# Performance work log

Hardware: AMD Instinct MI355X
Metric: run time of the kernel (lower is better)

## Reference

```python
import jax, jax.numpy as jnp
import numpy as np

B, N, L, C = 4, 16, 192, 64
H = 128
ROW, COL = 16, 12  # L == ROW*COL, ROW >= COL
NUM = 2  # class_num


def setup_inputs() -> dict:
    key = jax.random.key(0)
    ks = jax.random.split(key, 12)
    s = 1.0 / np.sqrt(H).astype(np.float32)
    u = lambda k, shape: jax.random.uniform(k, shape, jnp.float32, -s, s)
    return {
        "x": jax.random.normal(ks[0], (B, N, L, C), jnp.float32),
        "pad_mask": jnp.ones((B, N), jnp.bool_),
        "fc3_w": u(ks[1], (H, C)), "fc3_b": u(ks[2], (H,)),
        "fc4_w": u(ks[3], (H, H)), "fc4_b": u(ks[4], (H,)),
        "W_enc": u(ks[5], (NUM, 6 * H, 3 * H)), "B_enc": u(ks[6], (NUM, 6 * H)),
        "fc1_w": u(ks[7], (NUM, 1, H)), "fc1_b": u(ks[8], (NUM, 1)),
        "fc2_w": u(ks[9], (NUM, 1, H)), "fc2_b": u(ks[10], (NUM, 1)),
    }


def _witran_encoder(a, W, Bb):
    # a: [COL*BN, slice_len, H] diagonally-shifted input; W: [6H, 3H]; Bb: [6H]
    RBN, slice_len, _ = a.shape
    BN = RBN // COL
    R = COL  # Water2sea_slice_num (after permute(2,0,1,3), slices run over col)
    slice_ids = jnp.arange(RBN) // BN
    xs = jnp.transpose(a, (1, 0, 2))  # [slice_len, RBN, H]

    def step(carry, inp):
        h_row, h_col = carry
        x_s, s = inp
        g = jnp.concatenate([h_row, h_col, x_s], axis=-1) @ W.T  # [RBN, 6H]
        # torch adds bias only to first batch*(s+1) rows, and only while s < slice_num
        mask = (slice_ids <= s) & (s < R)
        g = g + jnp.where(mask[:, None], Bb, jnp.zeros((), g.dtype))
        sig = jax.nn.sigmoid(g[:, : 4 * H])
        th = jnp.tanh(g[:, 4 * H:])
        u_r, o_r, u_c, o_c = jnp.split(sig, 4, axis=-1)
        i_r, i_c = jnp.split(th, 2, axis=-1)
        h_row = jnp.tanh((1 - u_r) * h_row + u_r * i_r) * o_r
        h_col = jnp.tanh((1 - u_c) * h_col + u_c * i_c) * o_c
        # saved pieces (only valid for late s; we keep the last, which is always valid)
        loc = jnp.clip(s - ROW + 1, 0, R - 1)
        row_save = jax.lax.dynamic_slice_in_dim(h_row, loc * BN, BN, axis=0)
        col_save = h_col[(R - 1) * BN:, :]  # save BEFORE roll, as in torch
        h_col = jnp.roll(h_col, BN, axis=0)
        return (h_row, h_col), (row_save, col_save)

    h0 = jnp.zeros((RBN, H), a.dtype)
    (_, _), (row_saves, col_saves) = jax.lax.scan(
        step, (h0, h0), (xs, jnp.arange(slice_len)))
    # last entries == hidden_row_all[:, -1, -1, :], hidden_col_all[:, -1, -1, :]
    return row_saves[-1], col_saves[-1]  # each [BN, H]


def reference(x, pad_mask, fc3_w, fc3_b, fc4_w, fc4_b, W_enc, B_enc,
              fc1_w, fc1_b, fc2_w, fc2_b):
    Bn, Nn = x.shape[0], x.shape[1]
    h = jax.nn.relu(x @ fc3_w.T + fc3_b) @ fc4_w.T + fc4_b  # [B,N,L,H]
    xr = h.reshape(-1, ROW, COL, H)          # [BN, row, col, H]
    inp = jnp.transpose(xr, (2, 0, 1, 3))    # [col, BN, row, H]
    slice_len = COL + ROW - 1
    # diagonal 'water2sea' shift: transfer[r, :, r:r+ROW] = inp[r]
    padded = jnp.pad(inp, ((0, 0), (0, 0), (0, COL - 1), (0, 0)))
    transfer = jax.vmap(lambda t, r: jnp.roll(t, r, axis=1))(padded, jnp.arange(COL))
    a = transfer.reshape(COL * Bn * Nn, slice_len, H)

    def per_class(W, Bb, f1w, f1b, f2w, f2b):
        row_last, col_last = _witran_encoder(a, W, Bb)
        # torch: row := hidden_col_all tail, col := hidden_row_all tail
        out = 0.5 * (col_last @ f1w.T + f1b) + 0.5 * (row_last @ f2w.T + f2b)
        return out[:, 0]  # [BN]

    y = jax.vmap(per_class)(W_enc, B_enc, fc1_w, fc1_b, fc2_w, fc2_b)  # [NUM, BN]
    return jnp.transpose(y).reshape(Bn, Nn, NUM)
```

## Files before the change

### kernel.cpp

```cpp
#include <hip/hip_runtime.h>

typedef _Float16 hf;
typedef _Float16 half2v __attribute__((ext_vector_type(2)));
typedef _Float16 half8 __attribute__((ext_vector_type(8)));
typedef float f32x4 __attribute__((ext_vector_type(4)));
typedef int int4v __attribute__((ext_vector_type(4)));

constexpr int Steps = 27;

constexpr int OFF_WX = 393216;
constexpr int OFF_F3 = 589824;
constexpr int OFF_F4 = 598016;
constexpr int OFF_XW = 614400;
constexpr int GST = 7;

__device__ __forceinline__ int aidx(int r, int k) {
  int blk = k >> 3;
  return r * 256 + (((blk ^ (r & 7)) & 31) << 3) + (k & 7);
}
__device__ __forceinline__ int hidx(int r, int k) {
  int blk = k >> 3;
  return r * 128 + (((blk ^ (r & 15)) & 15) << 3) + (k & 7);
}
__device__ __forceinline__ int xidx(int r, int k) {
  int blk = k >> 3;
  return r * 64 + (((blk ^ (r & 7)) & 7) << 3) + (k & 7);
}
__device__ __forceinline__ float sigmoidf_(float x) { return 1.0f / (1.0f + __expf(-x)); }
__device__ __forceinline__ float tanh_(float x) { return 1.0f - 2.0f / (__expf(2.0f * x) + 1.0f); }

__global__ __launch_bounds__(512) void prep(const float* __restrict__ fc3_w,
                                            const float* __restrict__ fc4_w,
                                            const float* __restrict__ W_enc,
                                            hf* __restrict__ wsh) {
  int idx = blockIdx.x * 512 + threadIdx.x;
  if (idx >= OFF_XW) return;
  float v;
  if (idx < OFF_WX) {
    int jj = idx & 7, lane = (idx >> 3) & 63, rest = idx >> 9;
    int ks = rest & 7; rest >>= 3;
    int j = rest % 3; rest /= 3;
    int wv = rest & 15, cls = rest >> 4;
    int gate = (wv < 8) ? (j < 2 ? j : 4) : (j < 2 ? j + 2 : 5);
    int n = gate * 128 + (wv & 7) * 16 + (lane & 15);
    int k = ks * 32 + ((lane >> 4) << 3) + jj;
    v = W_enc[(cls * 768 + n) * 384 + k];
  } else if (idx < OFF_F3) {
    int f = idx - OFF_WX;
    int j = f & 7, lane = (f >> 3) & 63, rest = f >> 9;
    int ks = rest & 3; rest >>= 2;
    int wv = rest & 7; rest >>= 3;
    int gate = rest % 6, cls = rest / 6;
    int n = gate * 128 + wv * 16 + (lane & 15);
    int k = 256 + ks * 32 + ((lane >> 4) << 3) + j;
    v = W_enc[(cls * 768 + n) * 384 + k];
  } else if (idx < OFF_F4) {
    int f = idx - OFF_F3;
    int j = f & 7, lane = (f >> 3) & 63, rest = f >> 9;
    int ks = rest & 1, wv = rest >> 1;
    int n = wv * 16 + (lane & 15), k = ks * 32 + ((lane >> 4) << 3) + j;
    v = fc3_w[n * 64 + k];
  } else {
    int f = idx - OFF_F4;
    int j = f & 7, lane = (f >> 3) & 63, rest = f >> 9;
    int ks = rest & 3, wv = rest >> 2;
    int n = wv * 16 + (lane & 15), k = ks * 32 + ((lane >> 4) << 3) + j;
    v = fc4_w[n * 128 + k];
  }
  wsh[idx] = (hf)v;
}

__global__ __launch_bounds__(512) void prelude(
    const float* __restrict__ x, const float* __restrict__ fc3_b, const float* __restrict__ fc4_b,
    const float* __restrict__ B_enc, const hf* __restrict__ wsh, hf* __restrict__ xWb) {
  const int t = threadIdx.x, lane = t & 63, wv = t >> 6;
  const int c16 = lane & 15, quad = lane >> 4;
  const int row0 = blockIdx.x * 64, bn = row0 / 192, l0 = row0 % 192;
  const int d = wv * 16 + c16;

  __shared__ __attribute__((aligned(16))) hf xA[64 * 64];
  __shared__ __attribute__((aligned(16))) hf hbuf[64 * 128];
  __shared__ __attribute__((aligned(16))) hf xout[64 * 768];
  __shared__ float actf[64];

  {
    int r = t >> 3, cb = (t & 7) * 8;
    const float* xp = x + (size_t)(row0 + r) * 64 + cb;
    f32x4 a = *(const f32x4*)xp, b = *(const f32x4*)(xp + 4);
    half8 h;
    h[0] = (hf)a.x; h[1] = (hf)a.y; h[2] = (hf)a.z; h[3] = (hf)a.w;
    h[4] = (hf)b.x; h[5] = (hf)b.y; h[6] = (hf)b.z; h[7] = (hf)b.w;
    *(half8*)&xA[xidx(r, cb)] = h;
  }
  if (t < 64) {
    int l = l0 + t;
    actf[t] = ((l / 12) + (l % 12)) < 12 ? 1.f : 0.f;
  }
  __syncthreads();

  {
    float b3v = fc3_b[d];
    half8 w0 = *(const half8*)(wsh + OFF_F3 + (wv * 2 + 0) * 512 + lane * 8);
    half8 w1 = *(const half8*)(wsh + OFF_F3 + (wv * 2 + 1) * 512 + lane * 8);
    f32x4 acc[4] = {{0, 0, 0, 0}, {0, 0, 0, 0}, {0, 0, 0, 0}, {0, 0, 0, 0}};
#pragma unroll
    for (int mt = 0; mt < 4; ++mt) {
      half8 a0 = *(const half8*)&xA[xidx(mt * 16 + c16, quad * 8)];
      half8 a1 = *(const half8*)&xA[xidx(mt * 16 + c16, 32 + quad * 8)];
      acc[mt] = __builtin_amdgcn_mfma_f32_16x16x32_f16(a0, w0, acc[mt], 0, 0, 0);
      acc[mt] = __builtin_amdgcn_mfma_f32_16x16x32_f16(a1, w1, acc[mt], 0, 0, 0);
    }
#pragma unroll
    for (int mt = 0; mt < 4; ++mt)
#pragma unroll
      for (int r = 0; r < 4; ++r)
        hbuf[hidx(mt * 16 + quad * 4 + r, d)] = (hf)fmaxf(acc[mt][r] + b3v, 0.f);
  }
  __syncthreads();

  {
    float b4v = fc4_b[d];
    half8 w4[4];
#pragma unroll
    for (int ks = 0; ks < 4; ++ks)
      w4[ks] = *(const half8*)(wsh + OFF_F4 + (wv * 4 + ks) * 512 + lane * 8);
    f32x4 acc[4] = {{0, 0, 0, 0}, {0, 0, 0, 0}, {0, 0, 0, 0}, {0, 0, 0, 0}};
#pragma unroll
    for (int mt = 0; mt < 4; ++mt)
#pragma unroll
      for (int ks = 0; ks < 4; ++ks) {
        half8 a = *(const half8*)&hbuf[hidx(mt * 16 + c16, ks * 32 + quad * 8)];
        acc[mt] = __builtin_amdgcn_mfma_f32_16x16x32_f16(a, w4[ks], acc[mt], 0, 0, 0);
      }
    __syncthreads();
#pragma unroll
    for (int mt = 0; mt < 4; ++mt)
#pragma unroll
      for (int r = 0; r < 4; ++r)
        hbuf[hidx(mt * 16 + quad * 4 + r, d)] = (hf)(acc[mt][r] + b4v);
  }
  __syncthreads();

  half8 af[4][4];
#pragma unroll
  for (int mt = 0; mt < 4; ++mt)
#pragma unroll
    for (int ks = 0; ks < 4; ++ks)
      af[mt][ks] = *(const half8*)&hbuf[hidx(mt * 16 + c16, ks * 32 + quad * 8)];

  for (int cls = 0; cls < 2; ++cls) {
    for (int g = 0; g < 6; ++g) {
      int pos = (g < 2) ? g : (g < 4 ? g + 1 : (g == 4 ? 2 : 5));
      half8 wf[4];
#pragma unroll
      for (int ks = 0; ks < 4; ++ks)
        wf[ks] = *(const half8*)(wsh + OFF_WX + (((cls * 6 + g) * 8 + wv) * 4 + ks) * 512 + lane * 8);
      float bv = B_enc[cls * 768 + g * 128 + d];
#pragma unroll
      for (int mt = 0; mt < 4; ++mt) {
        f32x4 acc = {0.f, 0.f, 0.f, 0.f};
#pragma unroll
        for (int ks = 0; ks < 4; ++ks)
          acc = __builtin_amdgcn_mfma_f32_16x16x32_f16(af[mt][ks], wf[ks], acc, 0, 0, 0);
#pragma unroll
        for (int r = 0; r < 4; ++r) {
          int row = mt * 16 + quad * 4 + r;
          xout[row * 768 + d * 6 + pos] = (hf)(acc[r] + actf[row] * bv);
        }
      }
    }
    __syncthreads();
    {
      const int* src = (const int*)xout;
      int* dst = (int*)(xWb + (((size_t)cls * 64 + bn) * 192 + l0) * 768);
#pragma unroll
      for (int i = 0; i < 12; ++i) {
        int base = (t + i * 512) * 4;
        *(int4v*)&dst[base] = *(const int4v*)&src[base];
      }
    }
    __syncthreads();
  }
}

__device__ __forceinline__ void xpre(const hf* __restrict__ xg, int t, int sN,
                                     unsigned* pa, unsigned* pb) {
#pragma unroll
  for (int i = 0; i < 3; ++i) {
    int u = t + (i << 10);
    int colf = u >= 1536;
    int q = colf ? u - 1536 : u;
    int c = q >> 7, dd = q & 127;
    int rr = sN - c;
    unsigned a = 0, b = 0;
    if (rr >= 0 && rr < 16) {
      const hf* p = xg + (size_t)(rr * 12 + c) * 768 + dd * 6;
      if (colf) {
        a = (unsigned)*(const unsigned short*)(p + 3);
        b = *(const unsigned*)(p + 4);
      } else {
        a = *(const unsigned*)p;
        b = (unsigned)*(const unsigned short*)(p + 2);
      }
    }
    pa[i] = a;
    pb[i] = b;
  }
}
__device__ __forceinline__ float lo16f(unsigned v) {
  return (float)__builtin_bit_cast(half2v, v)[0];
}
__device__ __forceinline__ float hi16f(unsigned v) {
  return (float)__builtin_bit_cast(half2v, v)[1];
}

__global__ __launch_bounds__(1024) __attribute__((amdgpu_waves_per_eu(4, 4))) void witran(
    const hf* __restrict__ wsh, const float* __restrict__ fc1_w, const float* __restrict__ fc1_b,
    const float* __restrict__ fc2_w, const float* __restrict__ fc2_b,
    const hf* __restrict__ xWb, float* __restrict__ out) {
  const int cls = blockIdx.x & 1, bn = blockIdx.x >> 1;
  const int t = threadIdx.x, lane = t & 63, wv = t >> 6;
  const int c16 = lane & 15, quad = lane >> 4;
  const int d = (wv & 7) * 16 + c16;
  const int goff = (wv < 8) ? 0 : 3;

  __shared__ __attribute__((aligned(16))) hf wlds[16 * 3072];
  __shared__ __attribute__((aligned(16))) hf A[2][4096];
  __shared__ float g_lds[12 * 128 * GST];
  __shared__ float red[128];

  for (int i = t; i < 4096; i += 1024) ((int*)A)[i] = 0;

  half8 wr[2][8], wr2[2];
  {
    const hf* wb = wsh + (((size_t)(cls * 16 + wv) * 3) * 8) * 512 + lane * 8;
#pragma unroll
    for (int ks = 0; ks < 8; ++ks) {
      wr[0][ks] = *(const half8*)(wb + ks * 512);
      wr[1][ks] = *(const half8*)(wb + (8 + ks) * 512);
    }
    wr2[0] = *(const half8*)(wb + 16 * 512);
    wr2[1] = *(const half8*)(wb + 17 * 512);
#pragma unroll
    for (int f = 0; f < 6; ++f)
      *(half8*)&wlds[wv * 3072 + f * 512 + lane * 8] = *(const half8*)(wb + (18 + f) * 512);
  }

  const hf* xg = xWb + ((size_t)cls * 64 + bn) * 192 * 768;

  unsigned pa[3], pb[3], na[3], nb[3];
  xpre(xg, t, 0, pa, pb);
  __syncthreads();

  for (int s = 0; s < Steps; ++s) {
    const hf* Ac = A[s & 1];
    hf* An = A[(s + 1) & 1];

    f32x4 a0 = {0, 0, 0, 0}, a1 = a0, a2 = a0;
#pragma unroll
    for (int ks = 0; ks < 8; ++ks) {
      half8 av = *(const half8*)&Ac[aidx(c16, ks * 32 + quad * 8)];
      a0 = __builtin_amdgcn_mfma_f32_16x16x32_f16(av, wr[0][ks], a0, 0, 0, 0);
      a1 = __builtin_amdgcn_mfma_f32_16x16x32_f16(av, wr[1][ks], a1, 0, 0, 0);
      half8 w2 = (ks < 2) ? wr2[ks]
                          : *(const half8*)&wlds[wv * 3072 + (ks - 2) * 512 + lane * 8];
      a2 = __builtin_amdgcn_mfma_f32_16x16x32_f16(av, w2, a2, 0, 0, 0);
    }
    if (quad < 3) {
#pragma unroll
      for (int r = 0; r < 4; ++r) {
        float* gp = &g_lds[((quad * 4 + r) * 128 + d) * GST + goff];
        gp[0] = a0[r];
        gp[1] = a1[r];
        gp[2] = a2[r];
      }
    }
    xpre(xg, t, s + 1, na, nb);
    __syncthreads();

#pragma unroll
    for (int i = 0; i < 3; ++i) {
      int u = t + (i << 10);
      int colf = u >= 1536;
      int q = colf ? u - 1536 : u;
      int c = q >> 7, dd = q & 127;
      if (c <= s) {
        const float* gp = &g_lds[(c * 128 + dd) * GST + (colf ? 3 : 0)];
        float xu, xo, xi;
        if (colf) {
          xu = lo16f(pa[i]); xo = lo16f(pb[i]); xi = hi16f(pb[i]);
        } else {
          xu = lo16f(pa[i]); xo = hi16f(pa[i]); xi = lo16f(pb[i]);
        }
        float gu = gp[0] + xu, go = gp[1] + xo, gi = gp[2] + xi;
        float hold = (float)Ac[aidx(c, colf ? 128 + dd : dd)];
        float uu = sigmoidf_(gu), oo = sigmoidf_(go), ii = tanh_(gi);
        float h = tanh_((1.f - uu) * hold + uu * ii) * oo;
        if (colf) {
          int c2 = (c == 11) ? 0 : c + 1;
          An[aidx(c2, 128 + dd)] = (hf)h;
        } else {
          An[aidx(c, dd)] = (hf)h;
        }
      }
    }
    __syncthreads();

#pragma unroll
    for (int i = 0; i < 3; ++i) { pa[i] = na[i]; pb[i] = nb[i]; }
  }

  if (t < 128) {
    float hr = (float)A[1][aidx(11, t)];
    float hc = (float)A[1][aidx(0, 128 + t)];
    red[t] = 0.5f * (hc * fc1_w[cls * 128 + t] + hr * fc2_w[cls * 128 + t]);
  }
  __syncthreads();
  if (t == 0) {
    float sum = 0.f;
    for (int i = 0; i < 128; ++i) sum += red[i];
    out[bn * 2 + cls] = sum + 0.5f * (fc1_b[cls] + fc2_b[cls]);
  }
}

extern "C" void kernel_launch(void* const* d_in, const int* in_sizes, int n_in,
                              void* d_out, int out_size, void* d_ws, size_t ws_size,
                              hipStream_t stream) {
  const float* x = (const float*)d_in[0];
  const float* fc3_w = (const float*)d_in[2];
  const float* fc3_b = (const float*)d_in[3];
  const float* fc4_w = (const float*)d_in[4];
  const float* fc4_b = (const float*)d_in[5];
  const float* W_enc = (const float*)d_in[6];
  const float* B_enc = (const float*)d_in[7];
  const float* fc1_w = (const float*)d_in[8];
  const float* fc1_b = (const float*)d_in[9];
  const float* fc2_w = (const float*)d_in[10];
  const float* fc2_b = (const float*)d_in[11];
  float* out = (float*)d_out;

  hf* wsh = (hf*)d_ws;
  hf* xWb = wsh + OFF_XW;

  prep<<<dim3(1200), dim3(512), 0, stream>>>(fc3_w, fc4_w, W_enc, wsh);
  prelude<<<dim3(192), dim3(512), 0, stream>>>(x, fc3_b, fc4_b, B_enc, wsh, xWb);
  witran<<<dim3(128), dim3(1024), 0, stream>>>(wsh, fc1_w, fc1_b, fc2_w, fc2_b, xWb, out);
}
```

Before: 194.9 us.

## Single-buffer hidden state, store gate pre-activations as fp16, move all third-gate weights to LDS

The hidden-state double buffer is replaced by a single buffer: each thread reads its old h into registers before the barrier and overwrites in place after it. Gate pre-activations are now staged in LDS as fp16 in a planar layout instead of fp32 with stride 7, which halves that traffic. All eight k-slices of the third weight set now come from LDS, so the wr2 registers go away. The next step's x prefetch is issued after the update instead of before the barrier. These changes cut LDS footprint and register pressure but add precision loss on the gates and make the prefetch latency less hidden.

After: 189.1 us. 3.0% less time.

```diff
diff --git a/kernel.cpp b/kernel.cpp
--- a/kernel.cpp
+++ b/kernel.cpp
@@ -12,7 +12,7 @@
 constexpr int OFF_F3 = 589824;
 constexpr int OFF_F4 = 598016;
 constexpr int OFF_XW = 614400;
-constexpr int GST = 7;
+constexpr int CST = 136;
 
 __device__ __forceinline__ int aidx(int r, int k) {
   int blk = k >> 3;
@@ -224,14 +224,14 @@
   const int d = (wv & 7) * 16 + c16;
   const int goff = (wv < 8) ? 0 : 3;
 
-  __shared__ __attribute__((aligned(16))) hf wlds[16 * 3072];
-  __shared__ __attribute__((aligned(16))) hf A[2][4096];
-  __shared__ float g_lds[12 * 128 * GST];
+  __shared__ __attribute__((aligned(16))) hf wlds[16 * 4096];
+  __shared__ __attribute__((aligned(16))) hf A[4096];
+  __shared__ hf g16[6 * 12 * CST];
   __shared__ float red[128];
 
-  for (int i = t; i < 4096; i += 1024) ((int*)A)[i] = 0;
-
-  half8 wr[2][8], wr2[2];
+  for (int i = t; i < 2048; i += 1024) ((int*)A)[i] = 0;
+
+  half8 wr[2][8];
   {
     const hf* wb = wsh + (((size_t)(cls * 16 + wv) * 3) * 8) * 512 + lane * 8;
 #pragma unroll
@@ -239,43 +239,45 @@
       wr[0][ks] = *(const half8*)(wb + ks * 512);
       wr[1][ks] = *(const half8*)(wb + (8 + ks) * 512);
     }
-    wr2[0] = *(const half8*)(wb + 16 * 512);
-    wr2[1] = *(const half8*)(wb + 17 * 512);
-#pragma unroll
-    for (int f = 0; f < 6; ++f)
-      *(half8*)&wlds[wv * 3072 + f * 512 + lane * 8] = *(const half8*)(wb + (18 + f) * 512);
+#pragma unroll
+    for (int f = 0; f < 8; ++f)
+      *(half8*)&wlds[wv * 4096 + f * 512 + lane * 8] = *(const half8*)(wb + (16 + f) * 512);
   }
 
   const hf* xg = xWb + ((size_t)cls * 64 + bn) * 192 * 768;
 
-  unsigned pa[3], pb[3], na[3], nb[3];
+  unsigned pa[3], pb[3];
   xpre(xg, t, 0, pa, pb);
   __syncthreads();
 
   for (int s = 0; s < Steps; ++s) {
-    const hf* Ac = A[s & 1];
-    hf* An = A[(s + 1) & 1];
-
     f32x4 a0 = {0, 0, 0, 0}, a1 = a0, a2 = a0;
 #pragma unroll
     for (int ks = 0; ks < 8; ++ks) {
-      half8 av = *(const half8*)&Ac[aidx(c16, ks * 32 + quad * 8)];
+      half8 av = *(const half8*)&A[aidx(c16, ks * 32 + quad * 8)];
       a0 = __builtin_amdgcn_mfma_f32_16x16x32_f16(av, wr[0][ks], a0, 0, 0, 0);
       a1 = __builtin_amdgcn_mfma_f32_16x16x32_f16(av, wr[1][ks], a1, 0, 0, 0);
-      half8 w2 = (ks < 2) ? wr2[ks]
-                          : *(const half8*)&wlds[wv * 3072 + (ks - 2) * 512 + lane * 8];
+      half8 w2 = *(const half8*)&wlds[wv * 4096 + ks * 512 + lane * 8];
       a2 = __builtin_amdgcn_mfma_f32_16x16x32_f16(av, w2, a2, 0, 0, 0);
     }
     if (quad < 3) {
 #pragma unroll
       for (int r = 0; r < 4; ++r) {
-        float* gp = &g_lds[((quad * 4 + r) * 128 + d) * GST + goff];
-        gp[0] = a0[r];
-        gp[1] = a1[r];
-        gp[2] = a2[r];
-      }
-    }
-    xpre(xg, t, s + 1, na, nb);
+        int base = (quad * 4 + r) * CST + d;
+        g16[(goff + 0) * 12 * CST + base] = (hf)a0[r];
+        g16[(goff + 1) * 12 * CST + base] = (hf)a1[r];
+        g16[(goff + 2) * 12 * CST + base] = (hf)a2[r];
+      }
+    }
+    float hold[3];
+#pragma unroll
+    for (int i = 0; i < 3; ++i) {
+      int u = t + (i << 10);
+      int colf = u >= 1536;
+      int q = colf ? u - 1536 : u;
+      int c = q >> 7, dd = q & 127;
+      hold[i] = (float)A[aidx(c, colf ? 128 + dd : dd)];
+    }
     __syncthreads();
 
 #pragma unroll
@@ -285,34 +287,34 @@
       int q = colf ? u - 1536 : u;
       int c = q >> 7, dd = q & 127;
       if (c <= s) {
-        const float* gp = &g_lds[(c * 128 + dd) * GST + (colf ? 3 : 0)];
+        int base = c * CST + dd;
+        int po = colf ? 3 : 0;
+        float gu = (float)g16[(po + 0) * 12 * CST + base];
+        float go = (float)g16[(po + 1) * 12 * CST + base];
+        float gi = (float)g16[(po + 2) * 12 * CST + base];
         float xu, xo, xi;
         if (colf) {
           xu = lo16f(pa[i]); xo = lo16f(pb[i]); xi = hi16f(pb[i]);
         } else {
           xu = lo16f(pa[i]); xo = hi16f(pa[i]); xi = lo16f(pb[i]);
         }
-        float gu = gp[0] + xu, go = gp[1] + xo, gi = gp[2] + xi;
-        float hold = (float)Ac[aidx(c, colf ? 128 + dd : dd)];
-        float uu = sigmoidf_(gu), oo = sigmoidf_(go), ii = tanh_(gi);
-        float h = tanh_((1.f - uu) * hold + uu * ii) * oo;
+        float uu = sigmoidf_(gu + xu), oo = sigmoidf_(go + xo), ii = tanh_(gi + xi);
+        float h = tanh_((1.f - uu) * hold[i] + uu * ii) * oo;
         if (colf) {
           int c2 = (c == 11) ? 0 : c + 1;
-          An[aidx(c2, 128 + dd)] = (hf)h;
+          A[aidx(c2, 128 + dd)] = (hf)h;
         } else {
-          An[aidx(c, dd)] = (hf)h;
+          A[aidx(c, dd)] = (hf)h;
         }
       }
     }
-    __syncthreads();
-
-#pragma unroll
-    for (int i = 0; i < 3; ++i) { pa[i] = na[i]; pb[i] = nb[i]; }
+    xpre(xg, t, s + 1, pa, pb);
+    __syncthreads();
   }
 
   if (t < 128) {
-    float hr = (float)A[1][aidx(11, t)];
-    float hc = (float)A[1][aidx(0, 128 + t)];
+    float hr = (float)A[aidx(11, t)];
+    float hc = (float)A[aidx(0, 128 + t)];
     red[t] = 0.5f * (hc * fc1_w[cls * 128 + t] + hr * fc2_w[cls * 128 + t]);
   }
   __syncthreads();
```

## Apply gate nonlinearities directly on MFMA accumulators, removing LDS staging and a barrier

Applied to the files above, without the earlier changes.

The recurrent cell update now runs in each wave on the MFMA accumulator registers, instead of writing gate pre-activations to a shared-memory buffer and redistributing them across all threads. This removes the g_lds round trip and one __syncthreads per step. In exchange the elementwise work runs only on 3 of 4 quads in each wave, which leaves lanes idle. All tanh-gate weights for the third MFMA now come from LDS, with no register-resident copy, to free registers.

Result: slower. 204.2 us (+4.7%).

```diff
diff --git a/kernel.cpp b/kernel.cpp
--- a/kernel.cpp
+++ b/kernel.cpp
@@ -12,7 +12,6 @@
 constexpr int OFF_F3 = 589824;
 constexpr int OFF_F4 = 598016;
 constexpr int OFF_XW = 614400;
-constexpr int GST = 7;
 
 __device__ __forceinline__ int aidx(int r, int k) {
   int blk = k >> 3;
@@ -28,6 +27,12 @@
 }
 __device__ __forceinline__ float sigmoidf_(float x) { return 1.0f / (1.0f + __expf(-x)); }
 __device__ __forceinline__ float tanh_(float x) { return 1.0f - 2.0f / (__expf(2.0f * x) + 1.0f); }
+__device__ __forceinline__ float lo16f(unsigned v) {
+  return (float)__builtin_bit_cast(half2v, v)[0];
+}
+__device__ __forceinline__ float hi16f(unsigned v) {
+  return (float)__builtin_bit_cast(half2v, v)[1];
+}
 
 __global__ __launch_bounds__(512) void prep(const float* __restrict__ fc3_w,
                                             const float* __restrict__ fc4_w,
@@ -183,18 +188,15 @@
   }
 }
 
-__device__ __forceinline__ void xpre(const hf* __restrict__ xg, int t, int sN,
-                                     unsigned* pa, unsigned* pb) {
-#pragma unroll
-  for (int i = 0; i < 3; ++i) {
-    int u = t + (i << 10);
-    int colf = u >= 1536;
-    int q = colf ? u - 1536 : u;
-    int c = q >> 7, dd = q & 127;
+__device__ __forceinline__ void xpre_w(const hf* __restrict__ xg, int colf, int quad, int d,
+                                       int sN, unsigned* pa, unsigned* pb) {
+#pragma unroll
+  for (int r = 0; r < 4; ++r) {
+    int c = quad * 4 + r;
     int rr = sN - c;
     unsigned a = 0, b = 0;
-    if (rr >= 0 && rr < 16) {
-      const hf* p = xg + (size_t)(rr * 12 + c) * 768 + dd * 6;
+    if (quad < 3 && rr >= 0 && rr < 16) {
+      const hf* p = xg + (size_t)(rr * 12 + c) * 768 + d * 6;
       if (colf) {
         a = (unsigned)*(const unsigned short*)(p + 3);
         b = *(const unsigned*)(p + 4);
@@ -203,15 +205,9 @@
         b = (unsigned)*(const unsigned short*)(p + 2);
       }
     }
-    pa[i] = a;
-    pb[i] = b;
-  }
-}
-__device__ __forceinline__ float lo16f(unsigned v) {
-  return (float)__builtin_bit_cast(half2v, v)[0];
-}
-__device__ __forceinline__ float hi16f(unsigned v) {
-  return (float)__builtin_bit_cast(half2v, v)[1];
+    pa[r] = a;
+    pb[r] = b;
+  }
 }
 
 __global__ __launch_bounds__(1024) __attribute__((amdgpu_waves_per_eu(4, 4))) void witran(
@@ -222,16 +218,15 @@
   const int t = threadIdx.x, lane = t & 63, wv = t >> 6;
   const int c16 = lane & 15, quad = lane >> 4;
   const int d = (wv & 7) * 16 + c16;
-  const int goff = (wv < 8) ? 0 : 3;
-
-  __shared__ __attribute__((aligned(16))) hf wlds[16 * 3072];
+  const int colf = (wv >= 8);
+
+  __shared__ __attribute__((aligned(16))) hf wlds[16 * 4096];
   __shared__ __attribute__((aligned(16))) hf A[2][4096];
-  __shared__ float g_lds[12 * 128 * GST];
   __shared__ float red[128];
 
   for (int i = t; i < 4096; i += 1024) ((int*)A)[i] = 0;
 
-  half8 wr[2][8], wr2[2];
+  half8 wr[2][8];
   {
     const hf* wb = wsh + (((size_t)(cls * 16 + wv) * 3) * 8) * 512 + lane * 8;
 #pragma unroll
@@ -239,17 +234,15 @@
       wr[0][ks] = *(const half8*)(wb + ks * 512);
       wr[1][ks] = *(const half8*)(wb + (8 + ks) * 512);
     }
-    wr2[0] = *(const half8*)(wb + 16 * 512);
-    wr2[1] = *(const half8*)(wb + 17 * 512);
-#pragma unroll
-    for (int f = 0; f < 6; ++f)
-      *(half8*)&wlds[wv * 3072 + f * 512 + lane * 8] = *(const half8*)(wb + (18 + f) * 512);
+#pragma unroll
+    for (int f = 0; f < 8; ++f)
+      *(half8*)&wlds[wv * 4096 + f * 512 + lane * 8] = *(const half8*)(wb + (16 + f) * 512);
   }
 
   const hf* xg = xWb + ((size_t)cls * 64 + bn) * 192 * 768;
 
-  unsigned pa[3], pb[3], na[3], nb[3];
-  xpre(xg, t, 0, pa, pb);
+  unsigned pa[4], pb[4], na[4], nb[4];
+  xpre_w(xg, colf, quad, d, 0, pa, pb);
   __syncthreads();
 
   for (int s = 0; s < Steps; ++s) {
@@ -262,52 +255,45 @@
       half8 av = *(const half8*)&Ac[aidx(c16, ks * 32 + quad * 8)];
       a0 = __builtin_amdgcn_mfma_f32_16x16x32_f16(av, wr[0][ks], a0, 0, 0, 0);
       a1 = __builtin_amdgcn_mfma_f32_16x16x32_f16(av, wr[1][ks], a1, 0, 0, 0);
-      half8 w2 = (ks < 2) ? wr2[ks]
-                          : *(const half8*)&wlds[wv * 3072 + (ks - 2) * 512 + lane * 8];
+      half8 w2 = *(const half8*)&wlds[wv * 4096 + ks * 512 + lane * 8];
       a2 = __builtin_amdgcn_mfma_f32_16x16x32_f16(av, w2, a2, 0, 0, 0);
     }
+
+    xpre_w(xg, colf, quad, d, s + 1, na, nb);
+
     if (quad < 3) {
 #pragma unroll
       for (int r = 0; r < 4; ++r) {
-        float* gp = &g_lds[((quad * 4 + r) * 128 + d) * GST + goff];
-        gp[0] = a0[r];
-        gp[1] = a1[r];
-        gp[2] = a2[r];
-      }
-    }
-    xpre(xg, t, s + 1, na, nb);
+        int c = quad * 4 + r;
+        if (c <= s) {
+          float xu, xo, xi;
+          if (colf) {
+            xu = lo16f(pa[r]);
+            xo = lo16f(pb[r]);
+            xi = hi16f(pb[r]);
+          } else {
+            xu = lo16f(pa[r]);
+            xo = hi16f(pa[r]);
+            xi = lo16f(pb[r]);
+          }
+          float uu = sigmoidf_(a0[r] + xu);
+          float oo = sigmoidf_(a1[r] + xo);
+          float ii = tanh_(a2[r] + xi);
+          float hold = (float)Ac[aidx(c, colf ? 128 + d : d)];
+          float h = tanh_((1.f - uu) * hold + uu * ii) * oo;
+          if (colf) {
+            int c2 = (c == 11) ? 0 : c + 1;
+            An[aidx(c2, 128 + d)] = (hf)h;
+          } else {
+            An[aidx(c, d)] = (hf)h;
+          }
+        }
+      }
+    }
     __syncthreads();
 
 #pragma unroll
-    for (int i = 0; i < 3; ++i) {
-      int u = t + (i << 10);
-      int colf = u >= 1536;
-      int q = colf ? u - 1536 : u;
-      int c = q >> 7, dd = q & 127;
-      if (c <= s) {
-        const float* gp = &g_lds[(c * 128 + dd) * GST + (colf ? 3 : 0)];
-        float xu, xo, xi;
-        if (colf) {
-          xu = lo16f(pa[i]); xo = lo16f(pb[i]); xi = hi16f(pb[i]);
-        } else {
-          xu = lo16f(pa[i]); xo = hi16f(pa[i]); xi = lo16f(pb[i]);
-        }
-        float gu = gp[0] + xu, go = gp[1] + xo, gi = gp[2] + xi;
-        float hold = (float)Ac[aidx(c, colf ? 128 + dd : dd)];
-        float uu = sigmoidf_(gu), oo = sigmoidf_(go), ii = tanh_(gi);
-        float h = tanh_((1.f - uu) * hold + uu * ii) * oo;
-        if (colf) {
-          int c2 = (c == 11) ? 0 : c + 1;
-          An[aidx(c2, 128 + dd)] = (hf)h;
-        } else {
-          An[aidx(c, dd)] = (hf)h;
-        }
-      }
-    }
-    __syncthreads();
-
-#pragma unroll
-    for (int i = 0; i < 3; ++i) { pa[i] = na[i]; pb[i] = nb[i]; }
+    for (int r = 0; r < 4; ++r) { pa[r] = na[r]; pb[r] = nb[r]; }
   }
 
   if (t < 128) {
```
